# Optimization experiments

Hardware: AMD Instinct MI355X
Metric: run time of the kernel (lower is better)

The kernel has to match this reference:

```python
import jax, jax.numpy as jnp
import numpy as np


def _layernorm(x, g, b, eps=1e-5):
    mu = jnp.mean(x, axis=-1, keepdims=True)
    var = jnp.var(x, axis=-1, keepdims=True)
    return (x - mu) * jax.lax.rsqrt(var + eps) * g + b


def _forward(x_real, x_imag, dt, conv_w, conv_b, spec_re, spec_im, lam_re, lam_im,
             dt_param, sigma, noise_r, noise_i, ln_g, ln_b, W1, b1, w2, b2,
             Jg_W, Jg_b, Rg_W, Rg_b):
    B, T, C, H, W = x_real.shape
    x = x_real + 1j * x_imag  # complex field [B,T,C,H,W]

    # ---- spatial mixer: 3x3 conv applied to real/imag parts (linear op) ----
    def conv(z):
        z2 = z.reshape(B * T, C, H, W)
        y = jax.lax.conv_general_dilated(z2, conv_w, (1, 1), 'SAME',
                                         dimension_numbers=('NCHW', 'OIHW', 'NCHW'))
        return (y + conv_b[None, :, None, None]).reshape(B, T, C, H, W)
    x = x + (conv(x.real) + 1j * conv(x.imag))

    # ---- spectral mixer: pointwise complex filter in FFT domain ----
    Xf = jnp.fft.fft2(x, axes=(-2, -1), norm='ortho')
    filt = (spec_re + 1j * spec_im)[None, None]  # [1,1,C,H,W]
    x = x + jnp.fft.ifft2(Xf * filt, axes=(-2, -1), norm='ortho')

    # ---- metriplectic propagator: diagonal SSM scan in rfft2 space ----
    dt_eff = dt * jax.nn.softplus(dt_param)          # [C]
    dt_scalar = dt_eff.mean()
    xs = jnp.concatenate([x.real, x.imag], axis=0)   # [2B,T,C,H,W]; B_out=2B
    u = jnp.fft.rfft2(xs, axes=(-2, -1), norm='ortho')  # [2B,T,C,H,Wf]
    lam = -jax.nn.softplus(lam_re) + 1j * lam_im     # stable poles, [C]
    A = jnp.exp(lam * dt_eff.astype(jnp.complex64))  # [C]
    A = jnp.broadcast_to(A[None, None, :, None, None], u.shape)

    def comb(e1, e2):  # first-order linear recurrence h_t = a_t h_{t-1} + u_t
        a1, u1 = e1
        a2, u2 = e2
        return (a1 * a2, a2 * u1 + u2)
    _, h = jax.lax.associative_scan(comb, (A, u), axis=1)

    xt = jnp.fft.irfft2(h, s=(H, W), axes=(-2, -1), norm='ortho')  # [2B,T,C,H,W] real
    x_temporal = xt[:B] + 1j * xt[B:]

    noise = (noise_r + 1j * noise_i) * sigma * jnp.sqrt(dt_scalar)
    x = x + x_temporal + noise

    # ---- Port-Hamiltonian layer on real||imag channel concat ----
    xp = jnp.transpose(x, (0, 1, 3, 4, 2))                  # [B,T,H,W,C]
    xc = jnp.concatenate([xp.real, xp.imag], axis=-1)       # [B,T,H,W,2C]
    D = 2 * C
    x_in = _layernorm(xc, ln_g, ln_b)
    # grads of potential H = sum(MLP(x_in)) wrt x_in
    pot = lambda z: (jax.nn.silu(z @ W1 + b1) @ w2 + b2).sum()
    grads = jax.grad(pot)(x_in)
    M = (x_in @ Jg_W + Jg_b).reshape(*xc.shape[:-1], D, D)
    Jm = M - jnp.swapaxes(M, -1, -2)
    P = (x_in @ Rg_W + Rg_b).reshape(*xc.shape[:-1], D, D)
    R = jnp.einsum('...ki,...kj->...ij', P, P) + 1e-4 * jnp.eye(D, dtype=xc.dtype)
    update = jnp.einsum('...ij,...j->...i', Jm - R, grads)
    x_ph = xc + update * dt_scalar

    # output: [B,T,2C,H,W]; real half = out.real, imag half = out.imag
    return jnp.transpose(x_ph, (0, 1, 4, 2, 3))


def setup_inputs() -> dict:
    key = jax.random.key(0)
    ks = jax.random.split(key, 16)
    B, T, C, H, W = 2, 8, 16, 64, 64
    D = 2 * C
    hid = D * 4
    f32 = jnp.float32
    rn = lambda k, s, sc=1.0: jax.random.normal(k, s, f32) * sc
    return dict(
        x_real=rn(ks[0], (B, T, C, H, W)),
        x_imag=rn(ks[1], (B, T, C, H, W)),
        dt=jnp.asarray(0.1, f32),
        conv_w=rn(ks[2], (C, C, 3, 3), 0.05),
        conv_b=jnp.zeros((C,), f32),
        spec_re=rn(ks[3], (C, H, W), 0.1),
        spec_im=rn(ks[4], (C, H, W), 0.1),
        lam_re=rn(ks[5], (C,)),
        lam_im=rn(ks[6], (C,)),
        dt_param=rn(ks[7], (C,)),
        sigma=jnp.asarray(0.01, f32),
        noise_r=rn(ks[8], (B, T, C, H, W)),
        noise_i=rn(ks[9], (B, T, C, H, W)),
        ln_g=jnp.ones((D,), f32),
        ln_b=jnp.zeros((D,), f32),
        W1=rn(ks[10], (D, hid), 0.1),
        b1=jnp.zeros((hid,), f32),
        w2=rn(ks[11], (hid,), 0.1),
        b2=jnp.asarray(0.0, f32),
        Jg_W=rn(ks[12], (D, D * D), 0.02),
        Jg_b=jnp.zeros((D * D,), f32),
        Rg_W=rn(ks[13], (D, D * D), 0.02),
        Rg_b=jnp.zeros((D * D,), f32),
    )


def reference(x_real, x_imag, dt, conv_w, conv_b, spec_re, spec_im, lam_re, lam_im,
              dt_param, sigma, noise_r, noise_i, ln_g, ln_b, W1, b1, w2, b2,
              Jg_W, Jg_b, Rg_W, Rg_b):
    return _forward(x_real, x_imag, dt, conv_w, conv_b, spec_re, spec_im, lam_re,
                    lam_im, dt_param, sigma, noise_r, noise_i, ln_g, ln_b, W1, b1,
                    w2, b2, Jg_W, Jg_b, Rg_W, Rg_b)
```

## Files before the change

### kernel.cpp

```cpp
#include <hip/hip_runtime.h>
#include <math.h>
#include <utility>

#define Bb 2
#define Tt 8
#define Cc 16
#define Hh 64
#define Ww 64
#define Dd 32
#define HID 128
#define NPIX 4096
#define NIMG 256

typedef unsigned short ushort_t;
typedef unsigned int uint_t;
typedef __attribute__((ext_vector_type(8))) short short8;
typedef __attribute__((ext_vector_type(4))) float f32x4;
union U16 { uint4 u; short8 s; };

__device__ __forceinline__ float sp_f(float x) {
    return (x > 20.f) ? x : log1pf(expf(x));
}

__device__ __forceinline__ ushort_t f2bf(float f) {
    uint_t u = __float_as_uint(f);
    uint_t r = (u + 0x7fffu + ((u >> 16) & 1u)) >> 16;
    return (ushort_t)r;
}
__device__ __forceinline__ float bf2f(ushort_t h) { return __uint_as_float(((uint_t)h) << 16); }

__device__ __forceinline__ uint_t packbf(float hi, float lo) {
    return __builtin_amdgcn_perm(__float_as_uint(hi), __float_as_uint(lo), 0x07060302u);
}
__device__ __forceinline__ uint4 synth8(const float* gf, float xs) {
    uint4 r;
    r.x = packbf(gf[1] * xs, gf[0] * xs);
    r.y = packbf(gf[3] * xs, gf[2] * xs);
    r.z = packbf(gf[5] * xs, gf[4] * xs);
    r.w = packbf(gf[7] * xs, gf[6] * xs);
    return r;
}
__device__ __forceinline__ void expand8(uint4 v, float* f) {
    f[0] = __uint_as_float(v.x << 16); f[1] = __uint_as_float(v.x & 0xffff0000u);
    f[2] = __uint_as_float(v.y << 16); f[3] = __uint_as_float(v.y & 0xffff0000u);
    f[4] = __uint_as_float(v.z << 16); f[5] = __uint_as_float(v.z & 0xffff0000u);
    f[6] = __uint_as_float(v.w << 16); f[7] = __uint_as_float(v.w & 0xffff0000u);
}

template <typename F, int... Is>
__device__ __forceinline__ void unroll_impl(F&& f, std::integer_sequence<int, Is...>) {
    (f(std::integral_constant<int, Is>{}), ...);
}
template <int N, typename F>
__device__ __forceinline__ void cunroll(F&& f) {
    unroll_impl(f, std::make_integer_sequence<int, N>{});
}

#define MFMA16(a, b, c) __builtin_amdgcn_mfma_f32_16x16x32_bf16((a), (b), (c), 0, 0, 0)

struct cpx { float r, i; };
__device__ __forceinline__ cpx cadd(cpx a, cpx b) { return {a.r + b.r, a.i + b.i}; }
__device__ __forceinline__ cpx csub(cpx a, cpx b) { return {a.r - b.r, a.i - b.i}; }
__device__ __forceinline__ cpx cmulw(cpx a, float wr, float wi) {
    return {a.r * wr - a.i * wi, a.r * wi + a.i * wr};
}
template<int S>
__device__ __forceinline__ cpx cmulSi(cpx a) {
    return {-(float)S * a.i, (float)S * a.r};
}
template<int S>
__device__ __forceinline__ void dft8(cpx* y) {
    const float C = 0.70710678118654752f;
    cpx t0 = cadd(y[0], y[4]), t1 = csub(y[0], y[4]);
    cpx t2 = cadd(y[2], y[6]), t3 = csub(y[2], y[6]);
    cpx e0 = cadd(t0, t2), e2 = csub(t0, t2);
    cpx t3i = cmulSi<S>(t3);
    cpx e1 = cadd(t1, t3i), e3 = csub(t1, t3i);
    cpx u0 = cadd(y[1], y[5]), u1 = csub(y[1], y[5]);
    cpx u2 = cadd(y[3], y[7]), u3 = csub(y[3], y[7]);
    cpx o0 = cadd(u0, u2), o2 = csub(u0, u2);
    cpx u3i = cmulSi<S>(u3);
    cpx o1 = cadd(u1, u3i), o3 = csub(u1, u3i);
    o1 = cmulw(o1, C, (float)S * C);
    o2 = cmulSi<S>(o2);
    o3 = cmulw(o3, -C, (float)S * C);
    y[0] = cadd(e0, o0); y[4] = csub(e0, o0);
    y[1] = cadd(e1, o1); y[5] = csub(e1, o1);
    y[2] = cadd(e2, o2); y[6] = csub(e2, o2);
    y[3] = cadd(e3, o3); y[7] = csub(e3, o3);
}

template<int S>
__device__ __forceinline__ void fft2d_r8(float* reM, float* imM,
                                         const float* twr, const float* twi, int tid) {
    int j = tid & 63, g = tid >> 6;
    {
        cpx y[8];
        #pragma unroll
        for (int n1 = 0; n1 < 8; ++n1) {
            int a = j * 65 + n1 * 8 + g;
            y[n1] = {reM[a], imM[a]};
        }
        dft8<S>(y);
        #pragma unroll
        for (int k1 = 0; k1 < 8; ++k1) {
            int m = (g * k1) & 63;
            cpx b = cmulw(y[k1], twr[m], twi[m]);
            int a = j * 65 + k1 * 8 + g;
            reM[a] = b.r; imM[a] = b.i;
        }
    }
    __syncthreads();
    {
        cpx y[8];
        #pragma unroll
        for (int n2 = 0; n2 < 8; ++n2) {
            int a = j * 65 + g * 8 + n2;
            y[n2] = {reM[a], imM[a]};
        }
        dft8<S>(y);
        __syncthreads();
        #pragma unroll
        for (int k2 = 0; k2 < 8; ++k2) {
            int a = j * 65 + g + k2 * 8;
            reM[a] = y[k2].r; imM[a] = y[k2].i;
        }
    }
    __syncthreads();
    {
        cpx y[8];
        #pragma unroll
        for (int n1 = 0; n1 < 8; ++n1) {
            int a = (n1 * 8 + g) * 65 + j;
            y[n1] = {reM[a], imM[a]};
        }
        dft8<S>(y);
        #pragma unroll
        for (int k1 = 0; k1 < 8; ++k1) {
            int m = (g * k1) & 63;
            cpx b = cmulw(y[k1], twr[m], twi[m]);
            int a = (k1 * 8 + g) * 65 + j;
            reM[a] = b.r; imM[a] = b.i;
        }
    }
    __syncthreads();
    {
        cpx y[8];
        #pragma unroll
        for (int n2 = 0; n2 < 8; ++n2) {
            int a = (g * 8 + n2) * 65 + j;
            y[n2] = {reM[a], imM[a]};
        }
        dft8<S>(y);
        __syncthreads();
        #pragma unroll
        for (int k2 = 0; k2 < 8; ++k2) {
            int a = (g + k2 * 8) * 65 + j;
            reM[a] = y[k2].r; imM[a] = y[k2].i;
        }
    }
    __syncthreads();
}

__global__ __launch_bounds__(256)
void k_conv(const float* __restrict__ xr, const float* __restrict__ xi,
            const float* __restrict__ cw, const float* __restrict__ cb,
            float2* __restrict__ x1,
            const float* __restrict__ JW, const float* __restrict__ Jb,
            const float* __restrict__ RW, const float* __restrict__ Rb,
            const float* __restrict__ W1, const float* __restrict__ dtp,
            const float* __restrict__ dt_param,
            ushort_t* __restrict__ B1f, ushort_t* __restrict__ B2f,
            ushort_t* __restrict__ w1n, ushort_t* __restrict__ w1t,
            float* __restrict__ dts_out) {
    __shared__ float sre[Cc][18][18];
    __shared__ float sim[Cc][18][18];
    __shared__ float swt[8 * 16 * 12];
    __shared__ float sb[8];
    int tid = threadIdx.x;
    if (blockIdx.x >= 512) {
        const int N1 = 33 * 2048, N2 = 33 * 1024, N3 = 4096;
        int i = (blockIdx.x - 512) * 256 + tid;
        for (; i < N1 + N2 + N3; i += 40 * 256) {
            if (i < N1) {
                int s = i / 2048; int r = i % 2048;
                int ch = r >> 9; int lane = (r >> 3) & 63; int e = i & 7;
                int n = ch * 16 + (lane & 15);
                int k = s * 32 + ((lane >> 4) << 3) + e;
                float v;
                if (k < 1024) {
                    int d = k >> 5, rr = k & 31;
                    if (n < 32) v = JW[d * 1024 + n * 32 + rr] - JW[d * 1024 + rr * 32 + n];
                    else        v = RW[d * 1024 + (n - 32) * 32 + rr];
                } else {
                    int rr = k - 1024;
                    if (n < 32) v = Jb[n * 32 + rr] - Jb[rr * 32 + n];
                    else        v = Rb[(n - 32) * 32 + rr];
                }
                B1f[i] = f2bf(v);
            } else if (i < N1 + N2) {
                int i2 = i - N1;
                int s = i2 / 1024; int r = i2 % 1024;
                int ch = r >> 9; int lane = (r >> 3) & 63; int e = i2 & 7;
                int n = ch * 16 + (lane & 15);
                int k = s * 32 + ((lane >> 4) << 3) + e;
                float v;
                if (k < 1024) {
                    int d = k >> 5, kk = k & 31;
                    v = RW[d * 1024 + kk * 32 + n];
                } else {
                    v = Rb[(k - 1024) * 32 + n];
                }
                B2f[i2] = f2bf(v);
            } else {
                int i3 = i - N1 - N2;
                int d = i3 >> 7, h = i3 & 127;
                ushort_t v = f2bf(W1[i3]);
                w1n[i3] = v;
                w1t[h * 32 + d] = v;
            }
        }
        if (blockIdx.x == 512 && tid == 0) {
            float s = 0.f;
            for (int c = 0; c < Cc; ++c) s += sp_f(dt_param[c]);
            dts_out[0] = dtp[0] * s * (1.f / Cc);
        }
        return;
    }
    int blk = blockIdx.x;
    int bt = blk >> 5;
    int sub = blk & 31;
    int tile = sub >> 1, cohalf = sub & 1;
    int ty0 = (tile >> 2) * 16, tx0 = (tile & 3) * 16;
    for (int i = tid; i < 8 * 16 * 9; i += 256) {
        int g = i / 9, k = i % 9;
        swt[g * 12 + k] = cw[cohalf * 8 * 144 + i];
    }
    if (tid < 8) sb[tid] = cb[cohalf * 8 + tid];
    for (int i = tid; i < Cc * 18 * 18; i += 256) {
        int ci = i / 324; int r = i % 324; int y = r / 18, x = r % 18;
        int gy = ty0 + y - 1, gx = tx0 + x - 1;
        float vr = 0.f, vi = 0.f;
        if (gy >= 0 && gy < Hh && gx >= 0 && gx < Ww) {
            int gidx = (bt * Cc + ci) * NPIX + gy * Ww + gx;
            vr = xr[gidx]; vi = xi[gidx];
        }
        sre[ci][y][x] = vr; sim[ci][y][x] = vi;
    }
    __syncthreads();
    int py = tid >> 4, px = tid & 15;
    int gy = ty0 + py, gx = tx0 + px;
    float ar[8], ai[8];
    #pragma unroll
    for (int oc = 0; oc < 8; ++oc) {
        int cg = cohalf * 8 + oc;
        ar[oc] = sre[cg][py + 1][px + 1] + sb[oc];
        ai[oc] = sim[cg][py + 1][px + 1] + sb[oc];
    }
    for (int ci = 0; ci < Cc; ++ci) {
        float nr[9], ni[9];
        #pragma unroll
        for (int dy = 0; dy < 3; ++dy)
            #pragma unroll
            for (int dx = 0; dx < 3; ++dx) {
                nr[dy * 3 + dx] = sre[ci][py + dy][px + dx];
                ni[dy * 3 + dx] = sim[ci][py + dy][px + dx];
            }
        #pragma unroll
        for (int oc = 0; oc < 8; ++oc) {
            const float* wp = &swt[(oc * 16 + ci) * 12];
            float4 w0 = *(const float4*)&wp[0];
            float4 w1 = *(const float4*)&wp[4];
            float w8 = wp[8];
            ar[oc] += w0.x * nr[0] + w0.y * nr[1] + w0.z * nr[2]
                    + w0.w * nr[3] + w1.x * nr[4] + w1.y * nr[5]
                    + w1.z * nr[6] + w1.w * nr[7] + w8 * nr[8];
            ai[oc] += w0.x * ni[0] + w0.y * ni[1] + w0.z * ni[2]
                    + w0.w * ni[3] + w1.x * ni[4] + w1.y * ni[5]
                    + w1.z * ni[6] + w1.w * ni[7] + w8 * ni[8];
        }
    }
    #pragma unroll
    for (int oc = 0; oc < 8; ++oc)
        x1[(bt * Cc + cohalf * 8 + oc) * NPIX + gy * Ww + gx] = make_float2(ar[oc], ai[oc]);
}

__global__ __launch_bounds__(512)
void k_fft_fwd(const float2* __restrict__ x1,
               const float* __restrict__ spec_re, const float* __restrict__ spec_im,
               float2* __restrict__ X2f) {
    int img = blockIdx.x;
    int c = img % Cc;
    int tid = threadIdx.x;
    __shared__ float re[64 * 65], im[64 * 65];
    __shared__ float twr[64], twi[64];
    if (tid < 64) {
        float ang = -0.098174770424681038798f * (float)tid;
        twr[tid] = cosf(ang); twi[tid] = sinf(ang);
    }
    const float2* src = x1 + (size_t)img * NPIX;
    for (int idx = tid; idx < NPIX; idx += 512) {
        int h = idx >> 6, w = idx & 63;
        float2 v = src[idx];
        re[h * 65 + w] = v.x; im[h * 65 + w] = v.y;
    }
    __syncthreads();
    fft2d_r8<-1>(re, im, twr, twi, tid);
    const float* fr = spec_re + c * NPIX;
    const float* fi = spec_im + c * NPIX;
    float2* dst = X2f + (size_t)img * NPIX;
    for (int idx = tid; idx < NPIX; idx += 512) {
        int h = idx >> 6, w = idx & 63;
        float xr_ = re[h * 65 + w], xi_ = im[h * 65 + w];
        float gr = 1.f + fr[idx], gi = fi[idx];
        dst[idx] = make_float2(xr_ * gr - xi_ * gi, xi_ * gr + xr_ * gi);
    }
}

__global__ __launch_bounds__(512)
void k_fft_inv(const float2* __restrict__ Z,
               const float* __restrict__ lam_re, const float* __restrict__ lam_im,
               const float* __restrict__ dt_param, const float* __restrict__ dtp,
               const float* __restrict__ noise_r, const float* __restrict__ noise_i,
               const float* __restrict__ sigma_p, const float* __restrict__ dts_p,
               float2* __restrict__ xf) {
    int img = blockIdx.x; int tid = threadIdx.x;
    int b = img >> 7, t = (img >> 4) & 7, c = img & 15;
    __shared__ float re[64 * 65], im[64 * 65];
    __shared__ float twr[64], twi[64];
    if (tid < 64) {
        float ang = 0.098174770424681038798f * (float)tid;
        twr[tid] = cosf(ang); twi[tid] = sinf(ang);
    }
    float dte = dtp[0] * sp_f(dt_param[c]);
    float ea = expf(-sp_f(lam_re[c]) * dte);
    float ph = lam_im[c] * dte;
    float A1r = ea * cosf(ph), A1i = ea * sinf(ph);
    int w = tid & 63;
    float sgn = (w == 0 || w == 32) ? 0.f : ((w > 32) ? -1.f : 1.f);

    float accr[8], acci[8];
    #pragma unroll
    for (int j = 0; j < 8; ++j) { accr[j] = 0.f; acci[j] = 0.f; }
    float Ar = 1.f, Ai = 0.f;
    for (int k = 0; k <= t; ++k) {
        const float2* Zk = Z + ((size_t)((b * Tt + (t - k)) * Cc + c)) * NPIX;
        float cr = Ar, ci = sgn * Ai;
        #pragma unroll
        for (int j = 0; j < 8; ++j) {
            float2 z = Zk[tid + j * 512];
            accr[j] += cr * z.x - ci * z.y;
            acci[j] += cr * z.y + ci * z.x;
        }
        float nr = Ar * A1r - Ai * A1i;
        Ai = Ar * A1i + Ai * A1r;
        Ar = nr;
    }
    const float2* Zt = Z + (size_t)img * NPIX;
    #pragma unroll
    for (int j = 0; j < 8; ++j) {
        int idx = tid + j * 512;
        int h = idx >> 6;
        float2 z = Zt[idx];
        re[h * 65 + w] = z.x + accr[j];
        im[h * 65 + w] = z.y + acci[j];
    }
    __syncthreads();
    fft2d_r8<1>(re, im, twr, twi, tid);
    float ns = sigma_p[0] * sqrtf(dts_p[0]);
    const float inv = 1.f / 4096.f;
    float2* dst = xf + (size_t)img * NPIX;
    const float* nr = noise_r + (size_t)img * NPIX;
    const float* ni = noise_i + (size_t)img * NPIX;
    for (int idx = tid; idx < NPIX; idx += 512) {
        int h = idx >> 6, ww = idx & 63;
        dst[idx] = make_float2(re[h * 65 + ww] * inv + ns * nr[idx],
                               im[h * 65 + ww] * inv + ns * ni[idx]);
    }
}

__global__ __launch_bounds__(256, 2)
void k_ph(const float2* __restrict__ field,
          const float* __restrict__ ln_g, const float* __restrict__ ln_b,
          const float* __restrict__ b1, const float* __restrict__ w2,
          const ushort_t* __restrict__ w1n, const ushort_t* __restrict__ w1t,
          const ushort_t* __restrict__ B1f, const ushort_t* __restrict__ B2f,
          const float* __restrict__ dts_p,
          float* __restrict__ out) {
    __shared__ ushort_t xin_s[128 * 40];
    __shared__ ushort_t g_s[128 * 40];
    __shared__ ushort_t pg_s[128 * 40];
    __shared__ ushort_t A_s[128 * 136] __attribute__((aligned(16)));

    int tid = threadIdx.x;
    int bt = blockIdx.x >> 5;
    int pix0 = (blockIdx.x & 31) << 7;

    int p = tid & 127, half = tid >> 7;
    const float2* fbase = field + ((size_t)bt * 16) * NPIX + pix0 + p;
    float2 xv[8];
    float s1 = 0.f, s2 = 0.f;
    #pragma unroll
    for (int j = 0; j < 8; ++j) {
        xv[j] = fbase[(half * 8 + j) * NPIX];
        s1 += xv[j].x + xv[j].y;
        s2 += xv[j].x * xv[j].x + xv[j].y * xv[j].y;
    }
    float2* red = (float2*)A_s;
    red[p * 2 + half] = make_float2(s1, s2);
    __syncthreads();
    float2 r0 = red[p * 2], r1 = red[p * 2 + 1];
    float mu = (r0.x + r1.x) * 0.03125f;
    float var = (r0.y + r1.y) * 0.03125f - mu * mu;
    float rs = rsqrtf(var + 1e-5f);
    #pragma unroll
    for (int j = 0; j < 8; ++j) {
        int cf = half * 8 + j;
        xin_s[p * 40 + cf]      = f2bf((xv[j].x - mu) * rs * ln_g[cf] + ln_b[cf]);
        xin_s[p * 40 + cf + 16] = f2bf((xv[j].y - mu) * rs * ln_g[cf + 16] + ln_b[cf + 16]);
    }
    __syncthreads();

    int lane = tid & 63, wv = tid >> 6;
    int quad = lane >> 4, l15 = lane & 15;
    const f32x4 zero4 = {0.f, 0.f, 0.f, 0.f};
    int m0 = wv * 32;

    f32x4 zacc[2][8];
    #pragma unroll
    for (int mt = 0; mt < 2; ++mt)
        #pragma unroll
        for (int nt = 0; nt < 8; ++nt) zacc[mt][nt] = zero4;
    U16 az[2];
    #pragma unroll
    for (int mt = 0; mt < 2; ++mt)
        az[mt].u = *(const uint4*)&xin_s[(m0 + mt * 16 + l15) * 40 + quad * 8];
    #pragma unroll
    for (int nt = 0; nt < 8; ++nt) {
        U16 bz;
        bz.u = *(const uint4*)&w1t[(nt * 16 + l15) * 32 + quad * 8];
        zacc[0][nt] = MFMA16(az[0].s, bz.s, zacc[0][nt]);
        zacc[1][nt] = MFMA16(az[1].s, bz.s, zacc[1][nt]);
    }
    #pragma unroll
    for (int nt = 0; nt < 8; ++nt) {
        int col = nt * 16 + l15;
        float b1v = b1[col], w2v = w2[col];
        #pragma unroll
        for (int mt = 0; mt < 2; ++mt) {
            #pragma unroll
            for (int r = 0; r < 4; ++r) {
                int row = m0 + mt * 16 + quad * 4 + r;
                float z = zacc[mt][nt][r] + b1v;
                float s = 1.f / (1.f + expf(-z));
                float t = s * (1.f + z * (1.f - s)) * w2v;
                A_s[row * 136 + col] = f2bf(t);
            }
        }
    }
    __syncthreads();

    f32x4 gacc[2][2];
    #pragma unroll
    for (int mt = 0; mt < 2; ++mt)
        #pragma unroll
        for (int nt = 0; nt < 2; ++nt) gacc[mt][nt] = zero4;
    #pragma unroll
    for (int q = 0; q < 4; ++q) {
        U16 ag[2];
        #pragma unroll
        for (int mt = 0; mt < 2; ++mt)
            ag[mt].u = *(const uint4*)&A_s[(m0 + mt * 16 + l15) * 136 + q * 32 + quad * 8];
        #pragma unroll
        for (int nt = 0; nt < 2; ++nt) {
            U16 bg;
            bg.u = *(const uint4*)&w1n[(nt * 16 + l15) * 128 + q * 32 + quad * 8];
            gacc[0][nt] = MFMA16(ag[0].s, bg.s, gacc[0][nt]);
            gacc[1][nt] = MFMA16(ag[1].s, bg.s, gacc[1][nt]);
        }
    }
    #pragma unroll
    for (int mt = 0; mt < 2; ++mt)
        #pragma unroll
        for (int nt = 0; nt < 2; ++nt)
            #pragma unroll
            for (int r = 0; r < 4; ++r)
                g_s[(m0 + mt * 16 + quad * 4 + r) * 40 + nt * 16 + l15] = f2bf(gacc[mt][nt][r]);
    __syncthreads();

    const ushort_t* xr0 = &xin_s[(m0 + l15) * 40];
    const ushort_t* xr1 = &xin_s[(m0 + 16 + l15) * 40];
    uint4 gvp0 = *(const uint4*)&g_s[(m0 + l15) * 40 + quad * 8];
    uint4 gvp1 = *(const uint4*)&g_s[(m0 + 16 + l15) * 40 + quad * 8];
    float gf0[8], gf1[8];
    expand8(gvp0, gf0);
    expand8(gvp1, gf1);
    const uint4* B1v = (const uint4*)B1f;
    const uint4* B2v = (const uint4*)B2f;

    uint4 br[2][4];
    #pragma unroll
    for (int pf = 0; pf < 2; ++pf)
        #pragma unroll
        for (int ch = 0; ch < 4; ++ch)
            br[pf][ch] = B1v[(pf * 4 + ch) * 64 + lane];
    f32x4 acc1[4][2];
    #pragma unroll
    for (int ch = 0; ch < 4; ++ch) { acc1[ch][0] = zero4; acc1[ch][1] = zero4; }
    cunroll<33>([&](auto Sc) {
        constexpr int s = Sc.value;
        constexpr int cur = s & 1;
        U16 a0, a1;
        if constexpr (s < 32) {
            float x0 = bf2f(xr0[s]);
            float x1 = bf2f(xr1[s]);
            a0.u = synth8(gf0, x0);
            a1.u = synth8(gf1, x1);
        } else {
            a0.u = gvp0; a1.u = gvp1;
        }
        #pragma unroll
        for (int ch = 0; ch < 4; ++ch) {
            U16 b; b.u = br[cur][ch];
            acc1[ch][0] = MFMA16(a0.s, b.s, acc1[ch][0]);
            acc1[ch][1] = MFMA16(a1.s, b.s, acc1[ch][1]);
        }
        if constexpr (s + 2 < 33) {
            #pragma unroll
            for (int ch = 0; ch < 4; ++ch)
                br[cur][ch] = B1v[((s + 2) * 4 + ch) * 64 + lane];
        }
    });
    #pragma unroll
    for (int mt = 0; mt < 2; ++mt)
        #pragma unroll
        for (int c2 = 0; c2 < 2; ++c2)
            #pragma unroll
            for (int r = 0; r < 4; ++r)
                pg_s[(m0 + mt * 16 + quad * 4 + r) * 40 + c2 * 16 + l15] =
                    f2bf(acc1[2 + c2][mt][r]);
    __syncthreads();

    uint4 pgp0 = *(const uint4*)&pg_s[(m0 + l15) * 40 + quad * 8];
    uint4 pgp1 = *(const uint4*)&pg_s[(m0 + 16 + l15) * 40 + quad * 8];
    float pgf0[8], pgf1[8];
    expand8(pgp0, pgf0);
    expand8(pgp1, pgf1);
    uint4 br2[2][2];
    #pragma unroll
    for (int pf = 0; pf < 2; ++pf) {
        br2[pf][0] = B2v[(pf * 2 + 0) * 64 + lane];
        br2[pf][1] = B2v[(pf * 2 + 1) * 64 + lane];
    }
    f32x4 acc2[2][2];
    acc2[0][0] = zero4; acc2[0][1] = zero4; acc2[1][0] = zero4; acc2[1][1] = zero4;
    cunroll<33>([&](auto Sc) {
        constexpr int s = Sc.value;
        constexpr int cur = s & 1;
        U16 a0, a1;
        if constexpr (s < 32) {
            float x0 = bf2f(xr0[s]);
            float x1 = bf2f(xr1[s]);
            a0.u = synth8(pgf0, x0);
            a1.u = synth8(pgf1, x1);
        } else {
            a0.u = pgp0; a1.u = pgp1;
        }
        #pragma unroll
        for (int ch = 0; ch < 2; ++ch) {
            U16 b; b.u = br2[cur][ch];
            acc2[ch][0] = MFMA16(a0.s, b.s, acc2[ch][0]);
            acc2[ch][1] = MFMA16(a1.s, b.s, acc2[ch][1]);
        }
        if constexpr (s + 2 < 33) {
            br2[cur][0] = B2v[((s + 2) * 2 + 0) * 64 + lane];
            br2[cur][1] = B2v[((s + 2) * 2 + 1) * 64 + lane];
        }
    });

    __syncthreads();
    float* upd = (float*)A_s;
    #pragma unroll
    for (int mt = 0; mt < 2; ++mt) {
        #pragma unroll
        for (int c2 = 0; c2 < 2; ++c2) {
            int col = c2 * 16 + l15;
            #pragma unroll
            for (int r = 0; r < 4; ++r) {
                int row = m0 + mt * 16 + quad * 4 + r;
                float gval = bf2f(g_s[row * 40 + col]);
                upd[row * 33 + col] = acc1[c2][mt][r] - acc2[c2][mt][r] - 1e-4f * gval;
            }
        }
    }
    __syncthreads();
    float dts = dts_p[0];
    #pragma unroll
    for (int cc = 0; cc < 16; ++cc) {
        int c = half * 16 + cc;
        float2 v = fbase[cc * NPIX];
        float xcv = half ? v.y : v.x;
        out[((size_t)bt * 32 + c) * NPIX + pix0 + p] = xcv + dts * upd[p * 33 + c];
    }
}

extern "C" void kernel_launch(void* const* d_in, const int* in_sizes, int n_in,
                              void* d_out, int out_size, void* d_ws, size_t ws_size,
                              hipStream_t stream) {
    const float* x_real   = (const float*)d_in[0];
    const float* x_imag   = (const float*)d_in[1];
    const float* dt       = (const float*)d_in[2];
    const float* conv_w   = (const float*)d_in[3];
    const float* conv_b   = (const float*)d_in[4];
    const float* spec_re  = (const float*)d_in[5];
    const float* spec_im  = (const float*)d_in[6];
    const float* lam_re   = (const float*)d_in[7];
    const float* lam_im   = (const float*)d_in[8];
    const float* dt_param = (const float*)d_in[9];
    const float* sigma    = (const float*)d_in[10];
    const float* noise_r  = (const float*)d_in[11];
    const float* noise_i  = (const float*)d_in[12];
    const float* ln_g     = (const float*)d_in[13];
    const float* ln_b     = (const float*)d_in[14];
    const float* W1       = (const float*)d_in[15];
    const float* b1       = (const float*)d_in[16];
    const float* w2       = (const float*)d_in[17];
    const float* Jg_W     = (const float*)d_in[19];
    const float* Jg_b     = (const float*)d_in[20];
    const float* Rg_W     = (const float*)d_in[21];
    const float* Rg_b     = (const float*)d_in[22];

    float2* wsA = (float2*)d_ws;
    float2* wsB = wsA + 1048576;

    ushort_t* B1f = (ushort_t*)(wsB + 1048576);
    ushort_t* B2f = B1f + 33 * 2048;
    ushort_t* w1n = B2f + 33 * 1024;
    ushort_t* w1t = w1n + 4096;
    float*    dts = (float*)(w1t + 4096);

    k_conv<<<552, 256, 0, stream>>>(x_real, x_imag, conv_w, conv_b, wsA,
                                    Jg_W, Jg_b, Rg_W, Rg_b, W1, dt, dt_param,
                                    B1f, B2f, w1n, w1t, dts);
    k_fft_fwd<<<NIMG, 512, 0, stream>>>(wsA, spec_re, spec_im, wsB);
    k_fft_inv<<<NIMG, 512, 0, stream>>>(wsB, lam_re, lam_im, dt_param, dt,
                                        noise_r, noise_i, sigma, dts, wsA);
    k_ph<<<512, 256, 0, stream>>>(wsA, ln_g, ln_b, b1, w2, w1n, w1t, B1f, B2f, dts,
                                  (float*)d_out);
}
```

Baseline: 182.6 us.

## Split PH hidden GEMM into halves, drop barriers, deepen weight prefetch

The hidden-layer GEMM chain in k_ph now runs in two 64-column halves. This halves the A_s shared buffer and the live zacc accumulators, and the launch bound rises from 2 to 3 blocks per SM. Two __syncthreads are removed because each wave only reads back the shared rows it wrote itself. The B1/B2 weight register prefetch goes from double to triple buffering to hide global load latency. The risks are more register pressure from the deeper prefetch against the tighter occupancy target, and possible spills.

```diff
diff --git a/kernel.cpp b/kernel.cpp
--- a/kernel.cpp
+++ b/kernel.cpp
@@ -379,7 +379,7 @@
     }
 }
 
-__global__ __launch_bounds__(256, 2)
+__global__ __launch_bounds__(256, 3)
 void k_ph(const float2* __restrict__ field,
           const float* __restrict__ ln_g, const float* __restrict__ ln_b,
           const float* __restrict__ b1, const float* __restrict__ w2,
@@ -390,7 +390,7 @@
     __shared__ ushort_t xin_s[128 * 40];
     __shared__ ushort_t g_s[128 * 40];
     __shared__ ushort_t pg_s[128 * 40];
-    __shared__ ushort_t A_s[128 * 136] __attribute__((aligned(16)));
+    __shared__ ushort_t A_s[128 * 68] __attribute__((aligned(16)));
 
     int tid = threadIdx.x;
     int bt = blockIdx.x >> 5;
@@ -426,57 +426,59 @@
     const f32x4 zero4 = {0.f, 0.f, 0.f, 0.f};
     int m0 = wv * 32;
 
-    f32x4 zacc[2][8];
-    #pragma unroll
-    for (int mt = 0; mt < 2; ++mt)
-        #pragma unroll
-        for (int nt = 0; nt < 8; ++nt) zacc[mt][nt] = zero4;
     U16 az[2];
     #pragma unroll
     for (int mt = 0; mt < 2; ++mt)
         az[mt].u = *(const uint4*)&xin_s[(m0 + mt * 16 + l15) * 40 + quad * 8];
-    #pragma unroll
-    for (int nt = 0; nt < 8; ++nt) {
-        U16 bz;
-        bz.u = *(const uint4*)&w1t[(nt * 16 + l15) * 32 + quad * 8];
-        zacc[0][nt] = MFMA16(az[0].s, bz.s, zacc[0][nt]);
-        zacc[1][nt] = MFMA16(az[1].s, bz.s, zacc[1][nt]);
-    }
-    #pragma unroll
-    for (int nt = 0; nt < 8; ++nt) {
-        int col = nt * 16 + l15;
-        float b1v = b1[col], w2v = w2[col];
-        #pragma unroll
-        for (int mt = 0; mt < 2; ++mt) {
-            #pragma unroll
-            for (int r = 0; r < 4; ++r) {
-                int row = m0 + mt * 16 + quad * 4 + r;
-                float z = zacc[mt][nt][r] + b1v;
-                float s = 1.f / (1.f + expf(-z));
-                float t = s * (1.f + z * (1.f - s)) * w2v;
-                A_s[row * 136 + col] = f2bf(t);
+    f32x4 gacc[2][2];
+    #pragma unroll
+    for (int mt = 0; mt < 2; ++mt)
+        #pragma unroll
+        for (int nt = 0; nt < 2; ++nt) gacc[mt][nt] = zero4;
+    #pragma unroll
+    for (int hh = 0; hh < 2; ++hh) {
+        f32x4 zacc[2][4];
+        #pragma unroll
+        for (int mt = 0; mt < 2; ++mt)
+            #pragma unroll
+            for (int nt = 0; nt < 4; ++nt) zacc[mt][nt] = zero4;
+        #pragma unroll
+        for (int nt = 0; nt < 4; ++nt) {
+            U16 bz;
+            bz.u = *(const uint4*)&w1t[((hh * 4 + nt) * 16 + l15) * 32 + quad * 8];
+            zacc[0][nt] = MFMA16(az[0].s, bz.s, zacc[0][nt]);
+            zacc[1][nt] = MFMA16(az[1].s, bz.s, zacc[1][nt]);
+        }
+        #pragma unroll
+        for (int nt = 0; nt < 4; ++nt) {
+            int colg = (hh * 4 + nt) * 16 + l15;
+            int colh = nt * 16 + l15;
+            float b1v = b1[colg], w2v = w2[colg];
+            #pragma unroll
+            for (int mt = 0; mt < 2; ++mt) {
+                #pragma unroll
+                for (int r = 0; r < 4; ++r) {
+                    int row = m0 + mt * 16 + quad * 4 + r;
+                    float z = zacc[mt][nt][r] + b1v;
+                    float s = 1.f / (1.f + expf(-z));
+                    float t = s * (1.f + z * (1.f - s)) * w2v;
+                    A_s[row * 68 + colh] = f2bf(t);
+                }
             }
         }
-    }
-    __syncthreads();
-
-    f32x4 gacc[2][2];
-    #pragma unroll
-    for (int mt = 0; mt < 2; ++mt)
-        #pragma unroll
-        for (int nt = 0; nt < 2; ++nt) gacc[mt][nt] = zero4;
-    #pragma unroll
-    for (int q = 0; q < 4; ++q) {
-        U16 ag[2];
-        #pragma unroll
-        for (int mt = 0; mt < 2; ++mt)
-            ag[mt].u = *(const uint4*)&A_s[(m0 + mt * 16 + l15) * 136 + q * 32 + quad * 8];
-        #pragma unroll
-        for (int nt = 0; nt < 2; ++nt) {
-            U16 bg;
-            bg.u = *(const uint4*)&w1n[(nt * 16 + l15) * 128 + q * 32 + quad * 8];
-            gacc[0][nt] = MFMA16(ag[0].s, bg.s, gacc[0][nt]);
-            gacc[1][nt] = MFMA16(ag[1].s, bg.s, gacc[1][nt]);
+        #pragma unroll
+        for (int q = 0; q < 2; ++q) {
+            U16 ag[2];
+            #pragma unroll
+            for (int mt = 0; mt < 2; ++mt)
+                ag[mt].u = *(const uint4*)&A_s[(m0 + mt * 16 + l15) * 68 + q * 32 + quad * 8];
+            #pragma unroll
+            for (int nt = 0; nt < 2; ++nt) {
+                U16 bg;
+                bg.u = *(const uint4*)&w1n[(nt * 16 + l15) * 128 + hh * 64 + q * 32 + quad * 8];
+                gacc[0][nt] = MFMA16(ag[0].s, bg.s, gacc[0][nt]);
+                gacc[1][nt] = MFMA16(ag[1].s, bg.s, gacc[1][nt]);
+            }
         }
     }
     #pragma unroll
@@ -486,7 +488,6 @@
             #pragma unroll
             for (int r = 0; r < 4; ++r)
                 g_s[(m0 + mt * 16 + quad * 4 + r) * 40 + nt * 16 + l15] = f2bf(gacc[mt][nt][r]);
-    __syncthreads();
 
     const ushort_t* xr0 = &xin_s[(m0 + l15) * 40];
     const ushort_t* xr1 = &xin_s[(m0 + 16 + l15) * 40];
@@ -498,9 +499,9 @@
     const uint4* B1v = (const uint4*)B1f;
     const uint4* B2v = (const uint4*)B2f;
 
-    uint4 br[2][4];
-    #pragma unroll
-    for (int pf = 0; pf < 2; ++pf)
+    uint4 br[3][4];
+    #pragma unroll
+    for (int pf = 0; pf < 3; ++pf)
         #pragma unroll
         for (int ch = 0; ch < 4; ++ch)
             br[pf][ch] = B1v[(pf * 4 + ch) * 64 + lane];
@@ -509,7 +510,7 @@
     for (int ch = 0; ch < 4; ++ch) { acc1[ch][0] = zero4; acc1[ch][1] = zero4; }
     cunroll<33>([&](auto Sc) {
         constexpr int s = Sc.value;
-        constexpr int cur = s & 1;
+        constexpr int slot = s % 3;
         U16 a0, a1;
         if constexpr (s < 32) {
             float x0 = bf2f(xr0[s]);
@@ -521,14 +522,14 @@
         }
         #pragma unroll
         for (int ch = 0; ch < 4; ++ch) {
-            U16 b; b.u = br[cur][ch];
+            U16 b; b.u = br[slot][ch];
             acc1[ch][0] = MFMA16(a0.s, b.s, acc1[ch][0]);
             acc1[ch][1] = MFMA16(a1.s, b.s, acc1[ch][1]);
         }
-        if constexpr (s + 2 < 33) {
+        if constexpr (s + 3 < 33) {
             #pragma unroll
             for (int ch = 0; ch < 4; ++ch)
-                br[cur][ch] = B1v[((s + 2) * 4 + ch) * 64 + lane];
+                br[slot][ch] = B1v[((s + 3) * 4 + ch) * 64 + lane];
         }
     });
     #pragma unroll
@@ -539,16 +540,15 @@
             for (int r = 0; r < 4; ++r)
                 pg_s[(m0 + mt * 16 + quad * 4 + r) * 40 + c2 * 16 + l15] =
                     f2bf(acc1[2 + c2][mt][r]);
-    __syncthreads();
 
     uint4 pgp0 = *(const uint4*)&pg_s[(m0 + l15) * 40 + quad * 8];
     uint4 pgp1 = *(const uint4*)&pg_s[(m0 + 16 + l15) * 40 + quad * 8];
     float pgf0[8], pgf1[8];
     expand8(pgp0, pgf0);
     expand8(pgp1, pgf1);
-    uint4 br2[2][2];
-    #pragma unroll
-    for (int pf = 0; pf < 2; ++pf) {
+    uint4 br2[3][2];
+    #pragma unroll
+    for (int pf = 0; pf < 3; ++pf) {
         br2[pf][0] = B2v[(pf * 2 + 0) * 64 + lane];
         br2[pf][1] = B2v[(pf * 2 + 1) * 64 + lane];
     }
@@ -556,7 +556,7 @@
     acc2[0][0] = zero4; acc2[0][1] = zero4; acc2[1][0] = zero4; acc2[1][1] = zero4;
     cunroll<33>([&](auto Sc) {
         constexpr int s = Sc.value;
-        constexpr int cur = s & 1;
+        constexpr int slot = s % 3;
         U16 a0, a1;
         if constexpr (s < 32) {
             float x0 = bf2f(xr0[s]);
@@ -568,13 +568,13 @@
         }
         #pragma unroll
         for (int ch = 0; ch < 2; ++ch) {
-            U16 b; b.u = br2[cur][ch];
+            U16 b; b.u = br2[slot][ch];
             acc2[ch][0] = MFMA16(a0.s, b.s, acc2[ch][0]);
             acc2[ch][1] = MFMA16(a1.s, b.s, acc2[ch][1]);
         }
-        if constexpr (s + 2 < 33) {
-            br2[cur][0] = B2v[((s + 2) * 2 + 0) * 64 + lane];
-            br2[cur][1] = B2v[((s + 2) * 2 + 1) * 64 + lane];
+        if constexpr (s + 3 < 33) {
+            br2[slot][0] = B2v[((s + 3) * 2 + 0) * 64 + lane];
+            br2[slot][1] = B2v[((s + 3) * 2 + 1) * 64 + lane];
         }
     });
 
```

After: 182.8 us. Within noise of the previous version (+0.1%).
